# Kernel tuning notes

Measured on AMD Instinct MI355X. Metric: run time of the kernel, lower is better.

## Reference

```python
import jax, jax.numpy as jnp
import numpy as np


def setup_inputs() -> dict:
    key = jax.random.key(0)
    k_x, k_b = jax.random.split(key)
    B, C, H, W = 32, 512, 32, 32
    x = jax.random.normal(k_x, (B, C, H, W), dtype=jnp.float32)
    beta = jax.random.normal(k_b, (1,), dtype=jnp.float32)
    return {"x": x, "beta": beta}


def reference(x, beta):
    B, C, H, W = x.shape
    feat = x.reshape(B, C, H * W)                       # [B, C, N]
    # channel-channel Gram matrix: [B, C, C]
    attn = jnp.einsum('bcn,bdn->bcd', feat, feat)
    # DANet-style reversed scores: rowmax - score, then softmax over last dim
    attn = jnp.max(attn, axis=-1, keepdims=True) - attn
    attn = jax.nn.softmax(attn, axis=-1)
    feat_e = jnp.einsum('bcd,bdn->bcn', attn, feat).reshape(B, C, H, W)
    return beta * feat_e + x
```

## Files before the change

### kernel.cpp

```cpp
#include <hip/hip_runtime.h>
#include <math.h>

constexpr int B = 32, C = 512, N = 1024;

typedef float f32x4 __attribute__((ext_vector_type(4)));
typedef _Float16 f16x8 __attribute__((ext_vector_type(8)));
typedef unsigned short u16x4 __attribute__((ext_vector_type(4)));
typedef unsigned short u16x8 __attribute__((ext_vector_type(8)));

__device__ __forceinline__ unsigned short f32_to_f16u(float v) {
  union { _Float16 h; unsigned short u; } cv; cv.h = (_Float16)v; return cv.u;
}
__device__ __forceinline__ float f16u_to_f32(unsigned short u) {
  union { _Float16 h; unsigned short u; } cv; cv.u = u; return (float)cv.h;
}

__device__ __forceinline__ void glds16(const void* g, void* l) {
  __builtin_amdgcn_global_load_lds((const __attribute__((address_space(1))) void*)g,
                                   (__attribute__((address_space(3))) void*)l, 16, 0, 0);
}

__global__ __launch_bounds__(256) void convert_kernel(const float* __restrict__ x,
                                                      unsigned short* __restrict__ xf,
                                                      unsigned short* __restrict__ xfT) {
  const int b = blockIdx.z;
  const int cy = blockIdx.y * 64;
  const int nx = blockIdx.x * 64;
  const int t = threadIdx.x;
  const int r = t >> 4, c4 = (t & 15) * 4;

  __shared__ unsigned T[64][65];

#pragma unroll
  for (int rr = 0; rr < 64; rr += 16) {
    const int row = rr + r;
    const size_t gi = ((size_t)b * C + cy + row) * N + nx + c4;
    const float4 v = *(const float4*)&x[gi];
    u16x4 h;
    h[0] = f32_to_f16u(v.x); h[1] = f32_to_f16u(v.y);
    h[2] = f32_to_f16u(v.z); h[3] = f32_to_f16u(v.w);
    *(u16x4*)&xf[gi] = h;
    T[row][c4 + 0] = h[0]; T[row][c4 + 1] = h[1];
    T[row][c4 + 2] = h[2]; T[row][c4 + 3] = h[3];
  }
  __syncthreads();
#pragma unroll
  for (int rr = 0; rr < 64; rr += 16) {
    const int nrow = rr + r;
    u16x4 o;
    o[0] = (unsigned short)T[c4 + 0][nrow]; o[1] = (unsigned short)T[c4 + 1][nrow];
    o[2] = (unsigned short)T[c4 + 2][nrow]; o[3] = (unsigned short)T[c4 + 3][nrow];
    *(u16x4*)&xfT[((size_t)b * N + nx + nrow) * C + cy + c4] = o;
  }
}

__global__ __launch_bounds__(512, 2) void gram_soft_av(const unsigned short* __restrict__ xf,
                                                       const unsigned short* __restrict__ xfT,
                                                       const float* __restrict__ beta,
                                                       float* __restrict__ out) {
  const int l = blockIdx.x;
  const int xcd = l & 7, seq = l >> 3;
  const int b = xcd + 8 * (seq >> 3);
  const int i0 = (seq & 7) * 64;

  const unsigned short* __restrict__ Fh = xf  + (size_t)b * C * N;
  const unsigned short* __restrict__ FT = xfT + (size_t)b * N * C;
  float* __restrict__ ob = out + (size_t)b * C * N;

  __shared__ __align__(16) unsigned short Pb[4][512 * 32];
  unsigned short* Atile = &Pb[2][0];

  const int t = threadIdx.x, wave = t >> 6, lane = t & 63;
  const int lrow = lane & 15, quad = lane >> 4;
  const int srow = lane >> 2;
  const int sel  = ((lane & 3) ^ ((lane >> 3) & 3)) * 8;

  f32x4 acc[4][4] = {};

#define STAGE1(k0, nb)                                                    \
  {                                                                       \
    _Pragma("unroll")                                                     \
    for (int cc = 0; cc < 4; ++cc) {                                      \
      const int chunk = wave * 4 + cc;                                    \
      const int row = chunk * 16 + srow;                                  \
      glds16(Fh + (size_t)row * N + (k0) + sel, &Pb[nb][chunk * 512]);    \
    }                                                                     \
  }

  STAGE1(0, 0);
  STAGE1(32, 1);
  STAGE1(64, 2);

  for (int it = 0; it < 32; ++it) {
    const int k0 = it * 32;
    if (it < 30)       asm volatile("s_waitcnt vmcnt(8)" ::: "memory");
    else if (it == 30) asm volatile("s_waitcnt vmcnt(4)" ::: "memory");
    else               asm volatile("s_waitcnt vmcnt(0)" ::: "memory");
    __builtin_amdgcn_s_barrier();
    if (it + 3 < 32) STAGE1(k0 + 96, (it + 3) & 3);

    const unsigned short* __restrict__ Pc = Pb[it & 3];
    f16x8 ah[4], bh[4];
#pragma unroll
    for (int ti = 0; ti < 4; ++ti) {
      const int r = i0 + ti * 16 + lrow;
      ah[ti] = *(const f16x8*)&Pc[r * 32 + (quad ^ ((r >> 1) & 3)) * 8];
    }
#pragma unroll
    for (int tj = 0; tj < 4; ++tj) {
      const int r = wave * 64 + tj * 16 + lrow;
      bh[tj] = *(const f16x8*)&Pc[r * 32 + (quad ^ ((r >> 1) & 3)) * 8];
    }
    __builtin_amdgcn_s_setprio(1);
#pragma unroll
    for (int ti = 0; ti < 4; ++ti)
#pragma unroll
      for (int tj = 0; tj < 4; ++tj)
        acc[ti][tj] = __builtin_amdgcn_mfma_f32_16x16x32_f16(ah[ti], bh[tj], acc[ti][tj], 0, 0, 0);
    __builtin_amdgcn_s_setprio(0);
  }
#undef STAGE1

  __syncthreads();
  float* red = (float*)&Pb[0][0];
  float* fin = red + 512;

  float m[16];
#pragma unroll
  for (int ti = 0; ti < 4; ++ti)
#pragma unroll
    for (int rr = 0; rr < 4; ++rr)
      m[ti * 4 + rr] = fminf(fminf(acc[ti][0][rr], acc[ti][1][rr]),
                             fminf(acc[ti][2][rr], acc[ti][3][rr]));
#pragma unroll
  for (int o = 1; o < 16; o <<= 1)
#pragma unroll
    for (int s = 0; s < 16; ++s) m[s] = fminf(m[s], __shfl_xor(m[s], o, 64));
  if (lrow == 0)
#pragma unroll
    for (int ti = 0; ti < 4; ++ti)
#pragma unroll
      for (int rr = 0; rr < 4; ++rr)
        red[wave * 64 + ti * 16 + quad * 4 + rr] = m[ti * 4 + rr];
  __syncthreads();
  if (t < 64) {
    float v = red[t];
#pragma unroll
    for (int j = 1; j < 8; ++j) v = fminf(v, red[j * 64 + t]);
    fin[t] = v;
  }
  __syncthreads();

  float sm[16];
#pragma unroll
  for (int ti = 0; ti < 4; ++ti)
#pragma unroll
    for (int rr = 0; rr < 4; ++rr) {
      const float mn = fin[ti * 16 + quad * 4 + rr];
      float s = 0.f;
#pragma unroll
      for (int tj = 0; tj < 4; ++tj) {
        const float e = __expf(mn - acc[ti][tj][rr]);
        acc[ti][tj][rr] = e;
        s += e;
      }
      sm[ti * 4 + rr] = s;
    }
#pragma unroll
  for (int o = 1; o < 16; o <<= 1)
#pragma unroll
    for (int s = 0; s < 16; ++s) sm[s] += __shfl_xor(sm[s], o, 64);
  if (lrow == 0)
#pragma unroll
    for (int ti = 0; ti < 4; ++ti)
#pragma unroll
      for (int rr = 0; rr < 4; ++rr)
        red[wave * 64 + ti * 16 + quad * 4 + rr] = sm[ti * 4 + rr];
  __syncthreads();
  if (t < 64) {
    float v = 0.f;
#pragma unroll
    for (int j = 0; j < 8; ++j) v += red[j * 64 + t];
    fin[t] = 1.0f / v;
  }
  __syncthreads();

#pragma unroll
  for (int ti = 0; ti < 4; ++ti)
#pragma unroll
    for (int rr = 0; rr < 4; ++rr) {
      const float inv = fin[ti * 16 + quad * 4 + rr];
      const int rl = ti * 16 + quad * 4 + rr;
#pragma unroll
      for (int tj = 0; tj < 4; ++tj) {
        const int gcol = wave * 64 + tj * 16 + lrow;
        Atile[rl * 512 + ((((gcol >> 3) ^ (rl & 7)) << 3) | (gcol & 7))] =
            f32_to_f16u(acc[ti][tj][rr] * inv);
      }
    }
  __syncthreads();

  const float bv = beta[0];

  for (int jp = 0; jp < 2; ++jp) {
    f32x4 eacc[4][4] = {};
    u16x8 rsA[4];
#define LOADR_E(k0)                                                            \
    {                                                                          \
      _Pragma("unroll")                                                        \
      for (int cc = 0; cc < 4; ++cc) {                                         \
        const int chunk = wave * 4 + cc;                                       \
        const int row = chunk * 16 + srow;                                     \
        rsA[cc] = *(const u16x8*)&FT[(size_t)(jp * 512 + row) * C + (k0) + sel]; \
      }                                                                        \
    }
#define WRITER_E(nb)                                                           \
    {                                                                          \
      _Pragma("unroll")                                                        \
      for (int cc = 0; cc < 4; ++cc) {                                         \
        const int chunk = wave * 4 + cc;                                       \
        *(u16x8*)&Pb[nb][chunk * 512 + lane * 8] = rsA[cc];                    \
      }                                                                        \
    }
    LOADR_E(0);
    WRITER_E(0);
    LOADR_E(32);
    asm volatile("s_waitcnt lgkmcnt(0)" ::: "memory");
    __builtin_amdgcn_s_barrier();

    for (int it = 0; it < 16; ++it) {
      const int k0 = it * 32;
      const unsigned short* __restrict__ Pc = Pb[it & 1];
      f16x8 ah[4], bh[4];
#pragma unroll
      for (int ti = 0; ti < 4; ++ti) {
        const int ra = ti * 16 + lrow;
        ah[ti] = *(const f16x8*)&Atile[ra * 512 + ((((k0 >> 3) + quad) ^ (ra & 7)) << 3)];
      }
#pragma unroll
      for (int tj = 0; tj < 4; ++tj) {
        const int rb = wave * 64 + tj * 16 + lrow;
        bh[tj] = *(const f16x8*)&Pc[rb * 32 + ((quad ^ ((rb >> 1) & 3)) << 3)];
      }
      __builtin_amdgcn_s_setprio(1);
#pragma unroll
      for (int ti = 0; ti < 4; ++ti)
#pragma unroll
        for (int tj = 0; tj < 4; ++tj)
          eacc[ti][tj] = __builtin_amdgcn_mfma_f32_16x16x32_f16(ah[ti], bh[tj], eacc[ti][tj], 0, 0, 0);
      __builtin_amdgcn_s_setprio(0);

      if (it + 1 < 16) WRITER_E((it + 1) & 1);
      if (it + 2 < 16) LOADR_E(k0 + 64);
      asm volatile("s_waitcnt lgkmcnt(0)" ::: "memory");
      __builtin_amdgcn_s_barrier();
    }
#undef LOADR_E
#undef WRITER_E

    float* fs = (float*)&Pb[0][0] + wave * 1024;
#pragma unroll
    for (int ti = 0; ti < 4; ++ti) {
#pragma unroll
      for (int tj = 0; tj < 4; ++tj)
#pragma unroll
        for (int r = 0; r < 4; ++r)
          fs[(quad * 4 + r) * 64 + tj * 16 + lrow] = eacc[ti][tj][r];
      asm volatile("s_waitcnt lgkmcnt(0)" ::: "memory");
#pragma unroll
      for (int p = 0; p < 4; ++p) {
        const int f = p * 64 + lane;
        const int rr2 = f >> 4, cc4 = (f & 15) * 4;
        const f32x4 e = *(const f32x4*)&fs[rr2 * 64 + cc4];
        const int gr = i0 + ti * 16 + rr2;
        const int gc = jp * 512 + wave * 64 + cc4;
        const size_t o = (size_t)gr * N + gc;
        const u16x4 xv = *(const u16x4*)&Fh[o];
        f32x4 ov;
        ov[0] = fmaf(bv, e[0], f16u_to_f32(xv[0]));
        ov[1] = fmaf(bv, e[1], f16u_to_f32(xv[1]));
        ov[2] = fmaf(bv, e[2], f16u_to_f32(xv[2]));
        ov[3] = fmaf(bv, e[3], f16u_to_f32(xv[3]));
        __builtin_nontemporal_store(ov, (f32x4*)&ob[o]);
      }
    }
  }
}

extern "C" void kernel_launch(void* const* d_in, const int* in_sizes, int n_in,
                              void* d_out, int out_size, void* d_ws, size_t ws_size,
                              hipStream_t stream) {
  const float* x    = (const float*)d_in[0];
  const float* beta = (const float*)d_in[1];
  float* out = (float*)d_out;

  char* ws = (char*)d_ws;
  unsigned short* xf  = (unsigned short*)ws; ws += (size_t)B * C * N * 2;
  unsigned short* xfT = (unsigned short*)ws;

  convert_kernel<<<dim3(N / 64, C / 64, B), dim3(256), 0, stream>>>(x, xf, xfT);
  gram_soft_av  <<<dim3(256),               dim3(512), 0, stream>>>(xf, xfT, beta, out);
}
```

Before: 174.9 us.

## Double-buffer MFMA register fragments and deepen gram LDS pipeline to four stages

Both GEMM loops (Gram and attention-times-features) now prefetch the next iteration's LDS fragments into a second register set while the current MFMAs run. The loops are unrolled by two with ping-pong register buffers. The Gram stage also issues four global-to-LDS stages up front instead of three. This hides LDS read latency behind MFMA work. In exchange it uses more VGPRs, which may reduce occupancy or cause spills, and it adds an extra lgkmcnt wait in the epilogue.

Result: faster. 171.0 us (-2.3%).

```diff
diff --git a/kernel.cpp b/kernel.cpp
--- a/kernel.cpp
+++ b/kernel.cpp
@@ -87,38 +87,58 @@
     }                                                                     \
   }
 
+#define LOADFRAG1(AH, BH, jj)                                             \
+  {                                                                       \
+    const unsigned short* __restrict__ Pc = Pb[(jj) & 3];                 \
+    _Pragma("unroll")                                                     \
+    for (int ti = 0; ti < 4; ++ti) {                                      \
+      const int r = i0 + ti * 16 + lrow;                                  \
+      AH[ti] = *(const f16x8*)&Pc[r * 32 + (quad ^ ((r >> 1) & 3)) * 8];  \
+    }                                                                     \
+    _Pragma("unroll")                                                     \
+    for (int tj = 0; tj < 4; ++tj) {                                      \
+      const int r = wave * 64 + tj * 16 + lrow;                           \
+      BH[tj] = *(const f16x8*)&Pc[r * 32 + (quad ^ ((r >> 1) & 3)) * 8];  \
+    }                                                                     \
+  }
+
+#define MFMA16(AH, BH, ACC)                                               \
+  {                                                                       \
+    __builtin_amdgcn_s_setprio(1);                                        \
+    _Pragma("unroll")                                                     \
+    for (int ti = 0; ti < 4; ++ti)                                        \
+      _Pragma("unroll")                                                   \
+      for (int tj = 0; tj < 4; ++tj)                                      \
+        ACC[ti][tj] = __builtin_amdgcn_mfma_f32_16x16x32_f16(AH[ti], BH[tj], ACC[ti][tj], 0, 0, 0); \
+    __builtin_amdgcn_s_setprio(0);                                        \
+  }
+
+#define P1BODY(CA, CB, NA, NB, j)                                         \
+  {                                                                       \
+    if ((j) < 29)       asm volatile("s_waitcnt vmcnt(8) lgkmcnt(0)" ::: "memory"); \
+    else if ((j) == 29) asm volatile("s_waitcnt vmcnt(4) lgkmcnt(0)" ::: "memory"); \
+    else                asm volatile("s_waitcnt vmcnt(0) lgkmcnt(0)" ::: "memory"); \
+    __builtin_amdgcn_s_barrier();                                         \
+    if ((j) + 4 < 32) STAGE1(((j) + 4) * 32, ((j) + 4) & 3);              \
+    if ((j) + 1 < 32) LOADFRAG1(NA, NB, (j) + 1);                         \
+    MFMA16(CA, CB, acc);                                                  \
+  }
+
   STAGE1(0, 0);
   STAGE1(32, 1);
   STAGE1(64, 2);
-
-  for (int it = 0; it < 32; ++it) {
-    const int k0 = it * 32;
-    if (it < 30)       asm volatile("s_waitcnt vmcnt(8)" ::: "memory");
-    else if (it == 30) asm volatile("s_waitcnt vmcnt(4)" ::: "memory");
-    else               asm volatile("s_waitcnt vmcnt(0)" ::: "memory");
-    __builtin_amdgcn_s_barrier();
-    if (it + 3 < 32) STAGE1(k0 + 96, (it + 3) & 3);
-
-    const unsigned short* __restrict__ Pc = Pb[it & 3];
-    f16x8 ah[4], bh[4];
-#pragma unroll
-    for (int ti = 0; ti < 4; ++ti) {
-      const int r = i0 + ti * 16 + lrow;
-      ah[ti] = *(const f16x8*)&Pc[r * 32 + (quad ^ ((r >> 1) & 3)) * 8];
-    }
-#pragma unroll
-    for (int tj = 0; tj < 4; ++tj) {
-      const int r = wave * 64 + tj * 16 + lrow;
-      bh[tj] = *(const f16x8*)&Pc[r * 32 + (quad ^ ((r >> 1) & 3)) * 8];
-    }
-    __builtin_amdgcn_s_setprio(1);
-#pragma unroll
-    for (int ti = 0; ti < 4; ++ti)
-#pragma unroll
-      for (int tj = 0; tj < 4; ++tj)
-        acc[ti][tj] = __builtin_amdgcn_mfma_f32_16x16x32_f16(ah[ti], bh[tj], acc[ti][tj], 0, 0, 0);
-    __builtin_amdgcn_s_setprio(0);
-  }
+  STAGE1(96, 3);
+  asm volatile("s_waitcnt vmcnt(12)" ::: "memory");
+  __builtin_amdgcn_s_barrier();
+
+  f16x8 a0h[4], b0h[4], a1h[4], b1h[4];
+  LOADFRAG1(a0h, b0h, 0);
+
+  for (int j = 0; j < 32; j += 2) {
+    P1BODY(a0h, b0h, a1h, b1h, j);
+    P1BODY(a1h, b1h, a0h, b0h, j + 1);
+  }
+#undef P1BODY
 #undef STAGE1
 
   __syncthreads();
@@ -222,39 +242,44 @@
         *(u16x8*)&Pb[nb][chunk * 512 + lane * 8] = rsA[cc];                    \
       }                                                                        \
     }
+#define LOADFRAG2(AH, BH, uu)                                                  \
+    {                                                                          \
+      const unsigned short* __restrict__ Pc = Pb[(uu) & 1];                    \
+      const int kk = (uu) * 32;                                                \
+      _Pragma("unroll")                                                        \
+      for (int ti = 0; ti < 4; ++ti) {                                         \
+        const int ra = ti * 16 + lrow;                                         \
+        AH[ti] = *(const f16x8*)&Atile[ra * 512 + ((((kk >> 3) + quad) ^ (ra & 7)) << 3)]; \
+      }                                                                        \
+      _Pragma("unroll")                                                        \
+      for (int tj = 0; tj < 4; ++tj) {                                         \
+        const int rb = wave * 64 + tj * 16 + lrow;                             \
+        BH[tj] = *(const f16x8*)&Pc[rb * 32 + ((quad ^ ((rb >> 1) & 3)) << 3)]; \
+      }                                                                        \
+    }
+#define P2BODY(CA, CB, NA, NB, u)                                              \
+    {                                                                          \
+      if ((u) + 1 < 16) WRITER_E(((u) + 1) & 1);                               \
+      if ((u) + 2 < 16) LOADR_E(((u) + 2) * 32);                               \
+      asm volatile("s_waitcnt lgkmcnt(0)" ::: "memory");                       \
+      __builtin_amdgcn_s_barrier();                                            \
+      if ((u) + 1 < 16) LOADFRAG2(NA, NB, (u) + 1);                            \
+      MFMA16(CA, CB, eacc);                                                    \
+    }
+
     LOADR_E(0);
     WRITER_E(0);
     LOADR_E(32);
     asm volatile("s_waitcnt lgkmcnt(0)" ::: "memory");
     __builtin_amdgcn_s_barrier();
-
-    for (int it = 0; it < 16; ++it) {
-      const int k0 = it * 32;
-      const unsigned short* __restrict__ Pc = Pb[it & 1];
-      f16x8 ah[4], bh[4];
-#pragma unroll
-      for (int ti = 0; ti < 4; ++ti) {
-        const int ra = ti * 16 + lrow;
-        ah[ti] = *(const f16x8*)&Atile[ra * 512 + ((((k0 >> 3) + quad) ^ (ra & 7)) << 3)];
-      }
-#pragma unroll
-      for (int tj = 0; tj < 4; ++tj) {
-        const int rb = wave * 64 + tj * 16 + lrow;
-        bh[tj] = *(const f16x8*)&Pc[rb * 32 + ((quad ^ ((rb >> 1) & 3)) << 3)];
-      }
-      __builtin_amdgcn_s_setprio(1);
-#pragma unroll
-      for (int ti = 0; ti < 4; ++ti)
-#pragma unroll
-        for (int tj = 0; tj < 4; ++tj)
-          eacc[ti][tj] = __builtin_amdgcn_mfma_f32_16x16x32_f16(ah[ti], bh[tj], eacc[ti][tj], 0, 0, 0);
-      __builtin_amdgcn_s_setprio(0);
-
-      if (it + 1 < 16) WRITER_E((it + 1) & 1);
-      if (it + 2 < 16) LOADR_E(k0 + 64);
-      asm volatile("s_waitcnt lgkmcnt(0)" ::: "memory");
-      __builtin_amdgcn_s_barrier();
-    }
+    LOADFRAG2(a0h, b0h, 0);
+
+    for (int u = 0; u < 16; u += 2) {
+      P2BODY(a0h, b0h, a1h, b1h, u);
+      P2BODY(a1h, b1h, a0h, b0h, u + 1);
+    }
+#undef P2BODY
+#undef LOADFRAG2
 #undef LOADR_E
 #undef WRITER_E
 
@@ -283,8 +308,11 @@
         ov[3] = fmaf(bv, e[3], f16u_to_f32(xv[3]));
         __builtin_nontemporal_store(ov, (f32x4*)&ob[o]);
       }
-    }
-  }
+      asm volatile("s_waitcnt lgkmcnt(0)" ::: "memory");
+    }
+  }
+#undef MFMA16
+#undef LOADFRAG1
 }
 
 extern "C" void kernel_launch(void* const* d_in, const int* in_sizes, int n_in,
```

## Split MFMA loops into four barrier-separated phases interleaving LDS reads and loads

Applied to the files above, without the earlier changes.

Restructures both GEMM main loops (Gram and attention-times-features) into four phases per k-step. Each phase issues one A-fragment LDS read and a slice of the global prefetch, then runs four MFMAs between workgroup barriers, with sched_barrier used to pin the order. The Gram stage moves to a depth-4 prefetch and the second stage spreads its register loads and LDS writes across the phases. The aim is to interleave memory traffic with MFMA work in a ping-pong style, at the cost of many more s_barrier calls per iteration.

After: 182.5 us. 4.3% more time.

```diff
diff --git a/kernel.cpp b/kernel.cpp
--- a/kernel.cpp
+++ b/kernel.cpp
@@ -77,49 +77,78 @@
 
   f32x4 acc[4][4] = {};
 
-#define STAGE1(k0, nb)                                                    \
+#define BAR()   __builtin_amdgcn_s_barrier()
+#define LGKM0() asm volatile("s_waitcnt lgkmcnt(0)" ::: "memory"); \
+                __builtin_amdgcn_sched_barrier(0)
+
+#define RD_A1(DST, ti)                                                    \
+  { const int r = i0 + (ti) * 16 + lrow;                                  \
+    DST = *(const f16x8*)&Pc[r * 32 + (quad ^ ((r >> 1) & 3)) * 8]; }
+#define RD_B1(DST, tj)                                                    \
+  { const int r = wave * 64 + (tj) * 16 + lrow;                           \
+    DST = *(const f16x8*)&Pc[r * 32 + (quad ^ ((r >> 1) & 3)) * 8]; }
+#define G1(cc)                                                            \
+  if (j < 28) {                                                           \
+    const int row = (wave * 4 + (cc)) * 16 + srow;                        \
+    glds16(Fh + (size_t)row * N + k4 + sel, &Pb[nb4][(wave * 4 + (cc)) * 512]); \
+  }
+#define MF(p, AH, BH0, BH1, BH2, BH3, ACC)                                \
   {                                                                       \
-    _Pragma("unroll")                                                     \
-    for (int cc = 0; cc < 4; ++cc) {                                      \
-      const int chunk = wave * 4 + cc;                                    \
-      const int row = chunk * 16 + srow;                                  \
-      glds16(Fh + (size_t)row * N + (k0) + sel, &Pb[nb][chunk * 512]);    \
-    }                                                                     \
-  }
-
-  STAGE1(0, 0);
-  STAGE1(32, 1);
-  STAGE1(64, 2);
-
-  for (int it = 0; it < 32; ++it) {
-    const int k0 = it * 32;
-    if (it < 30)       asm volatile("s_waitcnt vmcnt(8)" ::: "memory");
-    else if (it == 30) asm volatile("s_waitcnt vmcnt(4)" ::: "memory");
-    else               asm volatile("s_waitcnt vmcnt(0)" ::: "memory");
-    __builtin_amdgcn_s_barrier();
-    if (it + 3 < 32) STAGE1(k0 + 96, (it + 3) & 3);
-
-    const unsigned short* __restrict__ Pc = Pb[it & 3];
-    f16x8 ah[4], bh[4];
-#pragma unroll
-    for (int ti = 0; ti < 4; ++ti) {
-      const int r = i0 + ti * 16 + lrow;
-      ah[ti] = *(const f16x8*)&Pc[r * 32 + (quad ^ ((r >> 1) & 3)) * 8];
-    }
-#pragma unroll
-    for (int tj = 0; tj < 4; ++tj) {
-      const int r = wave * 64 + tj * 16 + lrow;
-      bh[tj] = *(const f16x8*)&Pc[r * 32 + (quad ^ ((r >> 1) & 3)) * 8];
-    }
-    __builtin_amdgcn_s_setprio(1);
-#pragma unroll
-    for (int ti = 0; ti < 4; ++ti)
-#pragma unroll
-      for (int tj = 0; tj < 4; ++tj)
-        acc[ti][tj] = __builtin_amdgcn_mfma_f32_16x16x32_f16(ah[ti], bh[tj], acc[ti][tj], 0, 0, 0);
-    __builtin_amdgcn_s_setprio(0);
-  }
-#undef STAGE1
+    __builtin_amdgcn_s_setprio(1);                                        \
+    ACC[p][0] = __builtin_amdgcn_mfma_f32_16x16x32_f16(AH, BH0, ACC[p][0], 0, 0, 0); \
+    ACC[p][1] = __builtin_amdgcn_mfma_f32_16x16x32_f16(AH, BH1, ACC[p][1], 0, 0, 0); \
+    ACC[p][2] = __builtin_amdgcn_mfma_f32_16x16x32_f16(AH, BH2, ACC[p][2], 0, 0, 0); \
+    ACC[p][3] = __builtin_amdgcn_mfma_f32_16x16x32_f16(AH, BH3, ACC[p][3], 0, 0, 0); \
+    __builtin_amdgcn_s_setprio(0);                                        \
+  }
+
+  {
+#pragma unroll
+    for (int s = 0; s < 4; ++s)
+#pragma unroll
+      for (int cc = 0; cc < 4; ++cc) {
+        const int row = (wave * 4 + cc) * 16 + srow;
+        glds16(Fh + (size_t)row * N + s * 32 + sel, &Pb[s][(wave * 4 + cc) * 512]);
+      }
+    asm volatile("s_waitcnt vmcnt(12)" ::: "memory");
+    BAR();
+  }
+
+  for (int j = 0; j < 32; ++j) {
+    const unsigned short* __restrict__ Pc = Pb[j & 3];
+    const int k4 = (j + 4) * 32;
+    const int nb4 = (j + 4) & 3;
+    f16x8 bh0, bh1, bh2, bh3, ah;
+
+    RD_B1(bh0, 0); RD_B1(bh1, 1); RD_B1(bh2, 2); RD_B1(bh3, 3);
+    RD_A1(ah, 0);
+    G1(0);
+    BAR(); LGKM0();
+    MF(0, ah, bh0, bh1, bh2, bh3, acc);
+    BAR();
+    RD_A1(ah, 1);
+    G1(1);
+    BAR(); LGKM0();
+    MF(1, ah, bh0, bh1, bh2, bh3, acc);
+    BAR();
+    RD_A1(ah, 2);
+    G1(2);
+    BAR(); LGKM0();
+    MF(2, ah, bh0, bh1, bh2, bh3, acc);
+    BAR();
+    RD_A1(ah, 3);
+    if (j < 28)       asm volatile("s_waitcnt vmcnt(11)" ::: "memory");
+    else if (j == 28) asm volatile("s_waitcnt vmcnt(8)"  ::: "memory");
+    else if (j == 29) asm volatile("s_waitcnt vmcnt(4)"  ::: "memory");
+    else              asm volatile("s_waitcnt vmcnt(0)"  ::: "memory");
+    G1(3);
+    BAR(); LGKM0();
+    MF(3, ah, bh0, bh1, bh2, bh3, acc);
+    BAR();
+  }
+#undef G1
+#undef RD_A1
+#undef RD_B1
 
   __syncthreads();
   float* red = (float*)&Pb[0][0];
@@ -205,58 +234,60 @@
   for (int jp = 0; jp < 2; ++jp) {
     f32x4 eacc[4][4] = {};
     u16x8 rsA[4];
-#define LOADR_E(k0)                                                            \
+#define LOADR_E(k0, c0, c1)                                                    \
     {                                                                          \
-      _Pragma("unroll")                                                        \
-      for (int cc = 0; cc < 4; ++cc) {                                         \
-        const int chunk = wave * 4 + cc;                                       \
-        const int row = chunk * 16 + srow;                                     \
-        rsA[cc] = *(const u16x8*)&FT[(size_t)(jp * 512 + row) * C + (k0) + sel]; \
-      }                                                                        \
+      rsA[c0] = *(const u16x8*)&FT[(size_t)(jp * 512 + (wave * 4 + (c0)) * 16 + srow) * C + (k0) + sel]; \
+      rsA[c1] = *(const u16x8*)&FT[(size_t)(jp * 512 + (wave * 4 + (c1)) * 16 + srow) * C + (k0) + sel]; \
     }
 #define WRITER_E(nb)                                                           \
     {                                                                          \
       _Pragma("unroll")                                                        \
-      for (int cc = 0; cc < 4; ++cc) {                                         \
-        const int chunk = wave * 4 + cc;                                       \
-        *(u16x8*)&Pb[nb][chunk * 512 + lane * 8] = rsA[cc];                    \
-      }                                                                        \
-    }
-    LOADR_E(0);
+      for (int cc = 0; cc < 4; ++cc)                                           \
+        *(u16x8*)&Pb[nb][(wave * 4 + cc) * 512 + lane * 8] = rsA[cc];          \
+    }
+#define RD_A2(DST, ti)                                                         \
+    { const int ra = (ti) * 16 + lrow;                                         \
+      DST = *(const f16x8*)&Atile[ra * 512 + ((((kk >> 3) + quad) ^ (ra & 7)) << 3)]; }
+#define RD_B2(DST, tj)                                                         \
+    { const int rb = wave * 64 + (tj) * 16 + lrow;                             \
+      DST = *(const f16x8*)&Pc2[rb * 32 + ((quad ^ ((rb >> 1) & 3)) << 3)]; }
+
+    LOADR_E(0, 0, 1); LOADR_E(0, 2, 3);
     WRITER_E(0);
-    LOADR_E(32);
-    asm volatile("s_waitcnt lgkmcnt(0)" ::: "memory");
-    __builtin_amdgcn_s_barrier();
-
-    for (int it = 0; it < 16; ++it) {
-      const int k0 = it * 32;
-      const unsigned short* __restrict__ Pc = Pb[it & 1];
-      f16x8 ah[4], bh[4];
-#pragma unroll
-      for (int ti = 0; ti < 4; ++ti) {
-        const int ra = ti * 16 + lrow;
-        ah[ti] = *(const f16x8*)&Atile[ra * 512 + ((((k0 >> 3) + quad) ^ (ra & 7)) << 3)];
-      }
-#pragma unroll
-      for (int tj = 0; tj < 4; ++tj) {
-        const int rb = wave * 64 + tj * 16 + lrow;
-        bh[tj] = *(const f16x8*)&Pc[rb * 32 + ((quad ^ ((rb >> 1) & 3)) << 3)];
-      }
-      __builtin_amdgcn_s_setprio(1);
-#pragma unroll
-      for (int ti = 0; ti < 4; ++ti)
-#pragma unroll
-        for (int tj = 0; tj < 4; ++tj)
-          eacc[ti][tj] = __builtin_amdgcn_mfma_f32_16x16x32_f16(ah[ti], bh[tj], eacc[ti][tj], 0, 0, 0);
-      __builtin_amdgcn_s_setprio(0);
-
-      if (it + 1 < 16) WRITER_E((it + 1) & 1);
-      if (it + 2 < 16) LOADR_E(k0 + 64);
-      asm volatile("s_waitcnt lgkmcnt(0)" ::: "memory");
-      __builtin_amdgcn_s_barrier();
-    }
+    LOADR_E(32, 0, 1); LOADR_E(32, 2, 3);
+    LGKM0();
+    BAR();
+
+    for (int u = 0; u < 16; ++u) {
+      const unsigned short* __restrict__ Pc2 = Pb[u & 1];
+      const int kk = u * 32;
+      f16x8 bh0, bh1, bh2, bh3, ah;
+
+      RD_B2(bh0, 0); RD_B2(bh1, 1); RD_B2(bh2, 2); RD_B2(bh3, 3);
+      RD_A2(ah, 0);
+      BAR(); LGKM0();
+      MF(0, ah, bh0, bh1, bh2, bh3, eacc);
+      BAR();
+      RD_A2(ah, 1);
+      if (u + 1 < 16) WRITER_E((u + 1) & 1);
+      BAR(); LGKM0();
+      MF(1, ah, bh0, bh1, bh2, bh3, eacc);
+      BAR();
+      RD_A2(ah, 2);
+      if (u + 2 < 16) LOADR_E((u + 2) * 32, 0, 1);
+      BAR(); LGKM0();
+      MF(2, ah, bh0, bh1, bh2, bh3, eacc);
+      BAR();
+      RD_A2(ah, 3);
+      if (u + 2 < 16) LOADR_E((u + 2) * 32, 2, 3);
+      BAR(); LGKM0();
+      MF(3, ah, bh0, bh1, bh2, bh3, eacc);
+      BAR();
+    }
+#undef RD_B2
+#undef RD_A2
+#undef WRITER_E
 #undef LOADR_E
-#undef WRITER_E
 
     float* fs = (float*)&Pb[0][0] + wave * 1024;
 #pragma unroll
@@ -283,8 +314,12 @@
         ov[3] = fmaf(bv, e[3], f16u_to_f32(xv[3]));
         __builtin_nontemporal_store(ov, (f32x4*)&ob[o]);
       }
-    }
-  }
+      asm volatile("s_waitcnt lgkmcnt(0)" ::: "memory");
+    }
+  }
+#undef MF
+#undef BAR
+#undef LGKM0
 }
 
 extern "C" void kernel_launch(void* const* d_in, const int* in_sizes, int n_in,
```
